# Kernel optimization log

Measured on AMD Instinct MI355X. Metric: run time of the kernel, lower is better.

## Reference

```python
import jax, jax.numpy as jnp
import numpy as np

N_HEAD = 16
N_FEAT = 1024
D_K = N_FEAT // N_HEAD


def setup_inputs() -> dict:
    key = jax.random.key(0)
    ks = jax.random.split(key, 12)
    B, T, F = 4, 2048, N_FEAT
    s = 1.0 / np.sqrt(F)
    return {
        "query": jax.random.normal(ks[0], (B, T, F), dtype=jnp.float32),
        "key": jax.random.normal(ks[1], (B, T, F), dtype=jnp.float32),
        "value": jax.random.normal(ks[2], (B, T, F), dtype=jnp.float32),
        "mask": jnp.ones((B, 1, T), dtype=jnp.int32),
        "Wq": jax.random.normal(ks[3], (F, F), dtype=jnp.float32) * s,
        "bq": jax.random.normal(ks[4], (F,), dtype=jnp.float32) * 0.01,
        "Wk": jax.random.normal(ks[5], (F, F), dtype=jnp.float32) * s,
        "bk": jax.random.normal(ks[6], (F,), dtype=jnp.float32) * 0.01,
        "Wv": jax.random.normal(ks[7], (F, F), dtype=jnp.float32) * s,
        "bv": jax.random.normal(ks[8], (F,), dtype=jnp.float32) * 0.01,
        "Wo": jax.random.normal(ks[9], (F, F), dtype=jnp.float32) * s,
        "bo": jax.random.normal(ks[10], (F,), dtype=jnp.float32) * 0.01,
    }


def reference(query, key, value, mask, Wq, bq, Wk, bk, Wv, bv, Wo, bo):
    B, Tq, F = query.shape
    Tk = key.shape[1]
    h, dk = N_HEAD, D_K
    # torch nn.Linear: y = x @ W.T + b ; then view [B,T,h,dk] and transpose to [B,h,T,dk]
    q = (query @ Wq.T + bq).reshape(B, Tq, h, dk).transpose(0, 2, 1, 3)
    k = (key @ Wk.T + bk).reshape(B, Tk, h, dk).transpose(0, 2, 1, 3)
    v = (value @ Wv.T + bv).reshape(B, Tk, h, dk).transpose(0, 2, 1, 3)
    scale = 1.0 / np.sqrt(dk).astype(np.float32)
    scores = jnp.einsum("bhqd,bhkd->bhqk", q, k) * scale  # [B,h,Tq,Tk]
    # mask [B,1,Tk] -> unsqueeze(1) -> [B,1,1,Tk], True where mask == 0 (padded)
    pad = (mask[:, None, :, :] == 0)
    min_value = jnp.finfo(scores.dtype).min
    scores = jnp.where(pad, min_value, scores)
    atten = jax.nn.softmax(scores, axis=-1)
    atten = jnp.where(pad, 0.0, atten)
    # dropout_rate = 0.0 (eval): identity
    x = jnp.einsum("bhqk,bhkd->bhqd", atten, v)  # [B,h,Tq,dk]
    x = x.transpose(0, 2, 1, 3).reshape(B, Tq, h * dk)
    return x @ Wo.T + bo
```

## Files before the change

### kernel.cpp

```cpp
#include <hip/hip_runtime.h>
#include <hip/hip_bf16.h>


typedef unsigned short u16;
typedef unsigned long long u64;
typedef __attribute__((ext_vector_type(8))) short short8;
typedef __attribute__((ext_vector_type(4))) float f32x4;
typedef __attribute__((ext_vector_type(16))) float f32x16;
typedef __attribute__((ext_vector_type(4))) unsigned int u32x4;

#define GLOAD16(g, l) __builtin_amdgcn_global_load_lds( \
    (const __attribute__((address_space(1))) unsigned int*)(g), \
    (__attribute__((address_space(3))) unsigned int*)(l), 16, 0, 0)

__device__ __forceinline__ u16 f2bf(float x) {
  unsigned int u = __float_as_uint(x);
  return (u16)((u + 0x7fffu + ((u >> 16) & 1u)) >> 16);
}

__device__ __forceinline__ float fexp2(float x) {
#if __has_builtin(__builtin_amdgcn_exp2f)
  return __builtin_amdgcn_exp2f(x);
#else
  return exp2f(x);
#endif
}

__device__ __forceinline__ unsigned cvtpk(float lo, float hi) {
  unsigned r;
  asm("v_cvt_pk_bf16_f32 %0, %1, %2" : "=v"(r) : "v"(lo), "v"(hi));
  return r;
}

struct CvtArgs {
  const float* src[4];
  u16* dst[4];
};

__global__ __launch_bounds__(256) void cvt_multi(CvtArgs a, int shift) {
  const int id = blockIdx.x * 256 + threadIdx.x;
  const int seg = id >> shift;
  const int off = id & ((1 << shift) - 1);
  float4 v = ((const float4*)a.src[seg])[off];
  ushort4 o;
  o.x = f2bf(v.x); o.y = f2bf(v.y); o.z = f2bf(v.z); o.w = f2bf(v.w);
  ((ushort4*)a.dst[seg])[off] = o;
}

template <int EPI, int AF32>
__global__ __launch_bounds__(256) void gemm_bt(const void* __restrict__ Ap,
                                               const u16* __restrict__ Bw,
                                               const float* __restrict__ bias,
                                               void* __restrict__ Cout,
                                               float scale) {
  __shared__ __align__(16) char As[16384];
  __shared__ __align__(16) char Bs[16384];
  const int t = threadIdx.x;
  const int lane = t & 63;
  const int w = t >> 6;
  const int wm = w >> 1, wn = w & 1;
  const int l15 = lane & 15, l4 = lane >> 4;

  const int bid = blockIdx.x;
  const int swz = (bid & 7) * 64 + (bid >> 3);
  const int brow = swz >> 3;
  const int bcol = swz & 7;

  f32x4 acc[4][4] = {};

  const int srow = t >> 3;
  const int sbyte = (t & 7) * 16;
  const int arj = t >> 4;
  const int acol = t & 15;

  for (int kt = 0; kt < 16; ++kt) {
    const int k0 = kt * 64;
    __syncthreads();
    if constexpr (AF32) {
      const float* Ag = (const float*)Ap;
      float4 areg[8];
#pragma unroll
      for (int j = 0; j < 8; ++j)
        areg[j] = *(const float4*)(Ag + (size_t)(brow * 128 + j * 16 + arj) * 1024 +
                                   k0 + acol * 4);
#pragma unroll
      for (int i = 0; i < 4; ++i) {
        const int r = i * 32 + srow;
        const int sb = sbyte ^ ((r & 7) << 4);
        GLOAD16((const char*)(Bw + (size_t)(bcol * 128 + r) * 1024 + k0) + sb,
                Bs + i * 4096 + t * 16);
      }
#pragma unroll
      for (int j = 0; j < 8; ++j) {
        const int r = j * 16 + arj;
        uint2 pk = make_uint2(cvtpk(areg[j].x, areg[j].y), cvtpk(areg[j].z, areg[j].w));
        *(uint2*)(As + r * 128 + ((acol * 8) ^ ((r & 7) << 4))) = pk;
      }
    } else {
      const u16* Ag = (const u16*)Ap;
#pragma unroll
      for (int i = 0; i < 4; ++i) {
        const int r = i * 32 + srow;
        const int sb = sbyte ^ ((r & 7) << 4);
        GLOAD16((const char*)(Ag + (size_t)(brow * 128 + r) * 1024 + k0) + sb,
                As + i * 4096 + t * 16);
        GLOAD16((const char*)(Bw + (size_t)(bcol * 128 + r) * 1024 + k0) + sb,
                Bs + i * 4096 + t * 16);
      }
    }
    __syncthreads();
#pragma unroll
    for (int kf = 0; kf < 2; ++kf) {
      short8 af[4], bfv[4];
#pragma unroll
      for (int mi = 0; mi < 4; ++mi) {
        const int r = wm * 64 + mi * 16 + l15;
        af[mi] = *(const short8*)(As + r * 128 + ((kf * 64 + l4 * 16) ^ ((r & 7) << 4)));
      }
#pragma unroll
      for (int ni = 0; ni < 4; ++ni) {
        const int r = wn * 64 + ni * 16 + l15;
        bfv[ni] = *(const short8*)(Bs + r * 128 + ((kf * 64 + l4 * 16) ^ ((r & 7) << 4)));
      }
#pragma unroll
      for (int mi = 0; mi < 4; ++mi)
#pragma unroll
        for (int ni = 0; ni < 4; ++ni)
          acc[mi][ni] = __builtin_amdgcn_mfma_f32_16x16x32_bf16(
              af[mi], bfv[ni], acc[mi][ni], 0, 0, 0);
    }
  }

#pragma unroll
  for (int ni = 0; ni < 4; ++ni) {
    const int n = bcol * 128 + wn * 64 + ni * 16 + l15;
    const float bn = bias[n];
#pragma unroll
    for (int mi = 0; mi < 4; ++mi) {
      const int mb = brow * 128 + wm * 64 + mi * 16 + l4 * 4;
#pragma unroll
      for (int r = 0; r < 4; ++r) {
        const float v = acc[mi][ni][r] + bn;
        const int m = mb + r;
        const int b_ = m >> 11, tok = m & 2047, h_ = n >> 6, d = n & 63;
        if (EPI == 0) {
          ((u16*)Cout)[(((size_t)(b_ * 16 + h_) * 2048 + tok) << 6) + d] = f2bf(v * scale);
        } else if (EPI == 2) {
          ((u16*)Cout)[(((size_t)(b_ * 16 + h_) * 64 + d) << 11) + tok] = f2bf(v);
        } else {
          ((float*)Cout)[(size_t)m * 1024 + n] = v;
        }
      }
    }
  }
}

__global__ __launch_bounds__(256, 2) void attn_fwd5(const u16* __restrict__ Q,
                                                    const u16* __restrict__ Kp,
                                                    const u16* __restrict__ Vt,
                                                    const int* __restrict__ mask,
                                                    u16* __restrict__ ctx) {
  __shared__ u16 Ks[2][64 * 64];
  __shared__ u16 Vs[2][64 * 64];

  const int t = threadIdx.x, lane = t & 63, w = t >> 6;
  const int q31 = lane & 31, hi = lane >> 5;

  const int bid = blockIdx.x;
  const int swz = (bid & 7) * 64 + (bid >> 3);
  const int bh = swz >> 3;
  const int b_ = bh >> 4, h_ = bh & 15;
  const int q0 = (swz & 7) * 256 + w * 64;
  const size_t headO = (size_t)bh * 131072;

  short8 qfA[4], qfB[4];
  {
    const u16* qrowA = Q + headO + (size_t)(q0 + q31) * 64 + hi * 8;
    const u16* qrowB = qrowA + 32 * 64;
#pragma unroll
    for (int ds = 0; ds < 4; ++ds) {
      qfA[ds] = *(const short8*)(qrowA + ds * 16);
      qfB[ds] = *(const short8*)(qrowB + ds * 16);
    }
  }

  const int srow = t >> 3;
  const int sbyte = (t & 7) * 16;

#define STAGE_KV(bufi, kb)                                                      \
  {                                                                             \
    _Pragma("unroll") for (int i = 0; i < 2; ++i) {                             \
      const int r = i * 32 + srow;                                              \
      const int sb = sbyte ^ ((r & 7) << 4);                                    \
      GLOAD16((const char*)(Kp + headO + (size_t)((kb) + r) * 64) + sb,         \
              &Ks[bufi][(i * 4096 + t * 16) >> 1]);                             \
      GLOAD16((const char*)(Vt + headO + (size_t)r * 2048 + (kb)) + sb,         \
              &Vs[bufi][(i * 4096 + t * 16) >> 1]);                             \
    }                                                                           \
  }

#define PACK(sv, pfa, pfb)                                                      \
  {                                                                             \
    const unsigned w0 = cvtpk(sv[0], sv[1]),   w1 = cvtpk(sv[2], sv[3]);        \
    const unsigned w2 = cvtpk(sv[4], sv[5]),   w3 = cvtpk(sv[6], sv[7]);        \
    const unsigned w4 = cvtpk(sv[8], sv[9]),   w5 = cvtpk(sv[10], sv[11]);      \
    const unsigned w6 = cvtpk(sv[12], sv[13]), w7 = cvtpk(sv[14], sv[15]);      \
    const unsigned x0 = (unsigned)__shfl_xor((int)(hi ? w0 : w2), 32);          \
    const unsigned x1 = (unsigned)__shfl_xor((int)(hi ? w1 : w3), 32);          \
    const unsigned y0 = (unsigned)__shfl_xor((int)(hi ? w4 : w6), 32);          \
    const unsigned y1 = (unsigned)__shfl_xor((int)(hi ? w5 : w7), 32);          \
    u32x4 fa = hi ? (u32x4){x0, x1, w2, w3} : (u32x4){w0, w1, x0, x1};          \
    u32x4 fb = hi ? (u32x4){y0, y1, w6, w7} : (u32x4){w4, w5, y0, y1};          \
    pfa = __builtin_bit_cast(short8, fa);                                       \
    pfb = __builtin_bit_cast(short8, fb);                                       \
  }

  f32x16 oA0 = {}, oA1 = {}, oB0 = {}, oB1 = {};
  float lA = 0.f, lB = 0.f;
  const int kcol = hi * 16;
  const int rswz = (q31 & 7) << 4;

  STAGE_KV(0, 0);
  int mk = mask[b_ * 2048 + lane];
  __syncthreads();

  int buf = 0;
  for (int kt = 0; kt < 32; ++kt) {
    const int kb = kt * 64;
    if (kt + 1 < 32) STAGE_KV(buf ^ 1, kb + 64);
    const int mk_next = (kt + 1 < 32) ? mask[b_ * 2048 + kb + 64 + lane] : 0;
    const u64 bits = __ballot(mk != 0);

#pragma unroll
    for (int half = 0; half < 2; ++half) {
      f32x16 sA = {}, sB = {};
      __builtin_amdgcn_s_setprio(1);
#pragma unroll
      for (int ds = 0; ds < 4; ++ds) {
        const int byt = (half * 32 + q31) * 128 + ((ds * 32 + kcol) ^ rswz);
        short8 ka = *(const short8*)&Ks[buf][byt >> 1];
        sA = __builtin_amdgcn_mfma_f32_32x32x16_bf16(ka, qfA[ds], sA, 0, 0, 0);
        sB = __builtin_amdgcn_mfma_f32_32x32x16_bf16(ka, qfB[ds], sB, 0, 0, 0);
      }
      __builtin_amdgcn_s_setprio(0);

      if (bits == ~0ull) {
#pragma unroll
        for (int r = 0; r < 16; ++r) { sA[r] = fexp2(sA[r]); sB[r] = fexp2(sB[r]); }
      } else {
#pragma unroll
        for (int r = 0; r < 16; ++r) {
          const int k0 = half * 32 + (r & 3) + 8 * (r >> 2) + 4 * hi;
          const bool on = (bits >> k0) & 1;
          sA[r] = on ? fexp2(sA[r]) : 0.f;
          sB[r] = on ? fexp2(sB[r]) : 0.f;
        }
      }

      {
        float a0 = 0.f, a1 = 0.f, b0 = 0.f, b1 = 0.f;
#pragma unroll
        for (int r = 0; r < 16; r += 2) {
          a0 += sA[r]; a1 += sA[r + 1];
          b0 += sB[r]; b1 += sB[r + 1];
        }
        lA += a0 + a1;
        lB += b0 + b1;
      }

      short8 pA0, pA1, pB0, pB1;
      PACK(sA, pA0, pA1);
      PACK(sB, pB0, pB1);

      __builtin_amdgcn_s_setprio(1);
      {
        const int rb0 = q31 * 128, rb1 = (32 + q31) * 128;
        const int c0 = (half * 64 + kcol) ^ rswz;
        const int c1 = (half * 64 + 32 + kcol) ^ rswz;
        short8 va;
        va = *(const short8*)&Vs[buf][(rb0 + c0) >> 1];
        oA0 = __builtin_amdgcn_mfma_f32_32x32x16_bf16(va, pA0, oA0, 0, 0, 0);
        oB0 = __builtin_amdgcn_mfma_f32_32x32x16_bf16(va, pB0, oB0, 0, 0, 0);
        va = *(const short8*)&Vs[buf][(rb0 + c1) >> 1];
        oA0 = __builtin_amdgcn_mfma_f32_32x32x16_bf16(va, pA1, oA0, 0, 0, 0);
        oB0 = __builtin_amdgcn_mfma_f32_32x32x16_bf16(va, pB1, oB0, 0, 0, 0);
        va = *(const short8*)&Vs[buf][(rb1 + c0) >> 1];
        oA1 = __builtin_amdgcn_mfma_f32_32x32x16_bf16(va, pA0, oA1, 0, 0, 0);
        oB1 = __builtin_amdgcn_mfma_f32_32x32x16_bf16(va, pB0, oB1, 0, 0, 0);
        va = *(const short8*)&Vs[buf][(rb1 + c1) >> 1];
        oA1 = __builtin_amdgcn_mfma_f32_32x32x16_bf16(va, pA1, oA1, 0, 0, 0);
        oB1 = __builtin_amdgcn_mfma_f32_32x32x16_bf16(va, pB1, oB1, 0, 0, 0);
      }
      __builtin_amdgcn_s_setprio(0);
    }

    mk = mk_next;
    __syncthreads();
    buf ^= 1;
  }
#undef STAGE_KV

  lA += __shfl_xor(lA, 32);
  lB += __shfl_xor(lB, 32);
  const float invA = lA > 0.f ? 1.f / lA : 0.f;
  const float invB = lB > 0.f ? 1.f / lB : 0.f;
  const int tokA = q0 + q31;
  u16* crowA = ctx + ((size_t)b_ * 2048 + tokA) * 1024 + h_ * 64 + 4 * hi;
  u16* crowB = crowA + 32 * 1024;
#pragma unroll
  for (int g = 0; g < 4; ++g) {
    unsigned u0, u1;
    u0 = cvtpk(oA0[4 * g + 0] * invA, oA0[4 * g + 1] * invA);
    u1 = cvtpk(oA0[4 * g + 2] * invA, oA0[4 * g + 3] * invA);
    *(uint2*)(crowA + 8 * g) = make_uint2(u0, u1);
    u0 = cvtpk(oA1[4 * g + 0] * invA, oA1[4 * g + 1] * invA);
    u1 = cvtpk(oA1[4 * g + 2] * invA, oA1[4 * g + 3] * invA);
    *(uint2*)(crowA + 32 + 8 * g) = make_uint2(u0, u1);
    u0 = cvtpk(oB0[4 * g + 0] * invB, oB0[4 * g + 1] * invB);
    u1 = cvtpk(oB0[4 * g + 2] * invB, oB0[4 * g + 3] * invB);
    *(uint2*)(crowB + 8 * g) = make_uint2(u0, u1);
    u0 = cvtpk(oB1[4 * g + 0] * invB, oB1[4 * g + 1] * invB);
    u1 = cvtpk(oB1[4 * g + 2] * invB, oB1[4 * g + 3] * invB);
    *(uint2*)(crowB + 32 + 8 * g) = make_uint2(u0, u1);
  }
}

extern "C" void kernel_launch(void* const* d_in, const int* in_sizes, int n_in,
                              void* d_out, int out_size, void* d_ws, size_t ws_size,
                              hipStream_t stream) {
  const float* q_in = (const float*)d_in[0];
  const float* k_in = (const float*)d_in[1];
  const float* v_in = (const float*)d_in[2];
  const int*   mask = (const int*)d_in[3];
  const float* Wq = (const float*)d_in[4];
  const float* bq = (const float*)d_in[5];
  const float* Wk = (const float*)d_in[6];
  const float* bk = (const float*)d_in[7];
  const float* Wv = (const float*)d_in[8];
  const float* bv = (const float*)d_in[9];
  const float* Wo = (const float*)d_in[10];
  const float* bo = (const float*)d_in[11];
  float* out = (float*)d_out;

  char* ws = (char*)d_ws;
  u16* ctx = (u16*)(ws);
  u16* Qp = (u16*)(ws + 50331648);
  u16* Kp = (u16*)(ws + 67108864);
  u16* Vtb = (u16*)(ws + 83886080);
  u16* wqb = (u16*)(ws + 100663296);
  u16* wkb = (u16*)(ws + 102760448);
  u16* wvb = (u16*)(ws + 104857600);
  u16* wob = (u16*)(ws + 106954752);

  CvtArgs wts;
  wts.src[0] = Wq;  wts.src[1] = Wk;  wts.src[2] = Wv;  wts.src[3] = Wo;
  wts.dst[0] = wqb; wts.dst[1] = wkb; wts.dst[2] = wvb; wts.dst[3] = wob;
  cvt_multi<<<4 * 1024, 256, 0, stream>>>(wts, 18);

  const float C_SCALE = 0.18033688011112042f;
  gemm_bt<0, 1><<<512, 256, 0, stream>>>(q_in, wqb, bq, Qp, C_SCALE);
  gemm_bt<0, 1><<<512, 256, 0, stream>>>(k_in, wkb, bk, Kp, 1.0f);
  gemm_bt<2, 1><<<512, 256, 0, stream>>>(v_in, wvb, bv, Vtb, 1.0f);

  attn_fwd5<<<512, 256, 0, stream>>>(Qp, Kp, Vtb, mask, ctx);

  gemm_bt<1, 0><<<512, 256, 0, stream>>>(ctx, wob, bo, out, 1.0f);
}
```

Measured before the change: 217.6 us.

## Split attention over two key halves and combine partial outputs in a separate kernel

```diff
diff --git a/kernel.cpp b/kernel.cpp
--- a/kernel.cpp
+++ b/kernel.cpp
@@ -155,11 +155,12 @@
   }
 }
 
-__global__ __launch_bounds__(256, 2) void attn_fwd5(const u16* __restrict__ Q,
+__global__ __launch_bounds__(256, 2) void attn_fwd9(const u16* __restrict__ Q,
                                                     const u16* __restrict__ Kp,
                                                     const u16* __restrict__ Vt,
                                                     const int* __restrict__ mask,
-                                                    u16* __restrict__ ctx) {
+                                                    u16* __restrict__ Opart,
+                                                    float* __restrict__ lpart) {
   __shared__ u16 Ks[2][64 * 64];
   __shared__ u16 Vs[2][64 * 64];
 
@@ -167,10 +168,13 @@
   const int q31 = lane & 31, hi = lane >> 5;
 
   const int bid = blockIdx.x;
-  const int swz = (bid & 7) * 64 + (bid >> 3);
+  const int khalf = bid >> 9;
+  const int inner = bid & 511;
+  const int swz = (inner & 7) * 64 + (inner >> 3);
   const int bh = swz >> 3;
   const int b_ = bh >> 4, h_ = bh & 15;
   const int q0 = (swz & 7) * 256 + w * 64;
+  const int koff = khalf << 10;
   const size_t headO = (size_t)bh * 131072;
 
   short8 qfA[4], qfB[4];
@@ -220,15 +224,15 @@
   const int kcol = hi * 16;
   const int rswz = (q31 & 7) << 4;
 
-  STAGE_KV(0, 0);
-  int mk = mask[b_ * 2048 + lane];
+  STAGE_KV(0, koff);
+  int mk = mask[b_ * 2048 + koff + lane];
   __syncthreads();
 
   int buf = 0;
-  for (int kt = 0; kt < 32; ++kt) {
-    const int kb = kt * 64;
-    if (kt + 1 < 32) STAGE_KV(buf ^ 1, kb + 64);
-    const int mk_next = (kt + 1 < 32) ? mask[b_ * 2048 + kb + 64 + lane] : 0;
+  for (int kt = 0; kt < 16; ++kt) {
+    const int kb = koff + kt * 64;
+    if (kt + 1 < 16) STAGE_KV(buf ^ 1, kb + 64);
+    const int mk_next = (kt + 1 < 16) ? mask[b_ * 2048 + kb + 64 + lane] : 0;
     const u64 bits = __ballot(mk != 0);
 
 #pragma unroll
@@ -302,27 +306,64 @@
 
   lA += __shfl_xor(lA, 32);
   lB += __shfl_xor(lB, 32);
-  const float invA = lA > 0.f ? 1.f / lA : 0.f;
-  const float invB = lB > 0.f ? 1.f / lB : 0.f;
   const int tokA = q0 + q31;
-  u16* crowA = ctx + ((size_t)b_ * 2048 + tokA) * 1024 + h_ * 64 + 4 * hi;
+  u16* crowA = Opart + (size_t)khalf * 8388608 +
+               ((size_t)b_ * 2048 + tokA) * 1024 + h_ * 64 + 4 * hi;
   u16* crowB = crowA + 32 * 1024;
 #pragma unroll
   for (int g = 0; g < 4; ++g) {
     unsigned u0, u1;
-    u0 = cvtpk(oA0[4 * g + 0] * invA, oA0[4 * g + 1] * invA);
-    u1 = cvtpk(oA0[4 * g + 2] * invA, oA0[4 * g + 3] * invA);
+    u0 = cvtpk(oA0[4 * g + 0], oA0[4 * g + 1]);
+    u1 = cvtpk(oA0[4 * g + 2], oA0[4 * g + 3]);
     *(uint2*)(crowA + 8 * g) = make_uint2(u0, u1);
-    u0 = cvtpk(oA1[4 * g + 0] * invA, oA1[4 * g + 1] * invA);
-    u1 = cvtpk(oA1[4 * g + 2] * invA, oA1[4 * g + 3] * invA);
+    u0 = cvtpk(oA1[4 * g + 0], oA1[4 * g + 1]);
+    u1 = cvtpk(oA1[4 * g + 2], oA1[4 * g + 3]);
     *(uint2*)(crowA + 32 + 8 * g) = make_uint2(u0, u1);
-    u0 = cvtpk(oB0[4 * g + 0] * invB, oB0[4 * g + 1] * invB);
-    u1 = cvtpk(oB0[4 * g + 2] * invB, oB0[4 * g + 3] * invB);
+    u0 = cvtpk(oB0[4 * g + 0], oB0[4 * g + 1]);
+    u1 = cvtpk(oB0[4 * g + 2], oB0[4 * g + 3]);
     *(uint2*)(crowB + 8 * g) = make_uint2(u0, u1);
-    u0 = cvtpk(oB1[4 * g + 0] * invB, oB1[4 * g + 1] * invB);
-    u1 = cvtpk(oB1[4 * g + 2] * invB, oB1[4 * g + 3] * invB);
+    u0 = cvtpk(oB1[4 * g + 0], oB1[4 * g + 1]);
+    u1 = cvtpk(oB1[4 * g + 2], oB1[4 * g + 3]);
     *(uint2*)(crowB + 32 + 8 * g) = make_uint2(u0, u1);
   }
+  if (hi == 0) {
+    lpart[khalf * 131072 + bh * 2048 + tokA] = lA;
+    lpart[khalf * 131072 + bh * 2048 + tokA + 32] = lB;
+  }
+}
+
+__global__ __launch_bounds__(256) void combine_k(const u16* __restrict__ O0,
+                                                 const u16* __restrict__ O1,
+                                                 const float* __restrict__ lp,
+                                                 u16* __restrict__ ctx) {
+  const int i8 = blockIdx.x * 256 + threadIdx.x;
+  const int b = i8 >> 18;
+  const int tok = (i8 >> 7) & 2047;
+  const int h = (i8 >> 3) & 15;
+  const int bh = b * 16 + h;
+  const float l0 = lp[bh * 2048 + tok];
+  const float l1 = lp[131072 + bh * 2048 + tok];
+  const float ls = l0 + l1;
+  const float inv = ls > 0.f ? 1.f / ls : 0.f;
+
+  const uint4 a = ((const uint4*)O0)[i8];
+  const uint4 c = ((const uint4*)O1)[i8];
+  uint4 o;
+  {
+    unsigned au[4] = {a.x, a.y, a.z, a.w};
+    unsigned cu[4] = {c.x, c.y, c.z, c.w};
+    unsigned ou[4];
+#pragma unroll
+    for (int j = 0; j < 4; ++j) {
+      const float alo = __uint_as_float(au[j] << 16);
+      const float ahi = __uint_as_float(au[j] & 0xffff0000u);
+      const float clo = __uint_as_float(cu[j] << 16);
+      const float chi = __uint_as_float(cu[j] & 0xffff0000u);
+      ou[j] = cvtpk((alo + clo) * inv, (ahi + chi) * inv);
+    }
+    o.x = ou[0]; o.y = ou[1]; o.z = ou[2]; o.w = ou[3];
+  }
+  ((uint4*)ctx)[i8] = o;
 }
 
 extern "C" void kernel_launch(void* const* d_in, const int* in_sizes, int n_in,
@@ -344,6 +385,7 @@
 
   char* ws = (char*)d_ws;
   u16* ctx = (u16*)(ws);
+  u16* Op0 = (u16*)(ws + 16777216);
   u16* Qp = (u16*)(ws + 50331648);
   u16* Kp = (u16*)(ws + 67108864);
   u16* Vtb = (u16*)(ws + 83886080);
@@ -351,6 +393,7 @@
   u16* wkb = (u16*)(ws + 102760448);
   u16* wvb = (u16*)(ws + 104857600);
   u16* wob = (u16*)(ws + 106954752);
+  float* lpart = (float*)(ws + 100663296);
 
   CvtArgs wts;
   wts.src[0] = Wq;  wts.src[1] = Wk;  wts.src[2] = Wv;  wts.src[3] = Wo;
@@ -362,7 +405,9 @@
   gemm_bt<0, 1><<<512, 256, 0, stream>>>(k_in, wkb, bk, Kp, 1.0f);
   gemm_bt<2, 1><<<512, 256, 0, stream>>>(v_in, wvb, bv, Vtb, 1.0f);
 
-  attn_fwd5<<<512, 256, 0, stream>>>(Qp, Kp, Vtb, mask, ctx);
+  attn_fwd9<<<1024, 256, 0, stream>>>(Qp, Kp, Vtb, mask, Op0, lpart);
+
+  combine_k<<<4096, 256, 0, stream>>>(Op0, Op0 + 8388608, lpart, ctx);
 
   gemm_bt<1, 0><<<512, 256, 0, stream>>>(ctx, wob, bo, out, 1.0f);
 }
```

After: 234.1 us. 1.08x slower.
